# Optimization experiments

Hardware: AMD Instinct MI355X
Metric: run time of the kernel (lower is better)

## Reference

```python
import jax, jax.numpy as jnp
import numpy as np

N, C, H, W = 8, 32, 256, 256
DEPTH = 4
PAD = (1, 1, 2, 2, 1, 1)  # (w_l, w_r, h_t, h_b, d_f, d_b)
K = 2  # pool kernel/stride along each of D,H,W
EPS = 1e-5


def setup_inputs() -> dict:
    key = jax.random.key(0)
    k1, k2, k3, k4, k5 = jax.random.split(key, 5)
    x = jax.random.normal(k1, (N, C, H, W), dtype=jnp.float32)
    gamma = jax.random.normal(k2, (C,), dtype=jnp.float32) * 0.1 + 1.0
    beta = jax.random.normal(k3, (C,), dtype=jnp.float32) * 0.1
    conv_w = jax.random.normal(k4, (C, C), dtype=jnp.float32) / np.sqrt(C)  # 1x1 conv [out,in]
    conv_b = jax.random.normal(k5, (C,), dtype=jnp.float32) * 0.1
    return {"x": x, "gamma": gamma, "beta": beta, "conv_w": conv_w, "conv_b": conv_b}


def _forward(x, gamma, beta, conv_w, conv_b):
    n, c, h, w = x.shape
    # InstanceNorm2d (affine, biased variance, eps=1e-5), stats per (N,C) over H,W
    mean = jnp.mean(x, axis=(2, 3), keepdims=True)
    var = jnp.mean(jnp.square(x - mean), axis=(2, 3), keepdims=True)
    xn = (x - mean) * jax.lax.rsqrt(var + EPS)
    xn = xn * gamma[None, :, None, None] + beta[None, :, None, None]
    # expand to 5D by repeating along depth
    x3 = jnp.broadcast_to(xn[:, :, None, :, :], (n, c, DEPTH, h, w))
    # ConstantPad3d with value 0.0
    wl, wr, ht, hb, df, db = PAD
    xp = jnp.pad(x3, ((0, 0), (0, 0), (df, db), (ht, hb), (wl, wr)))
    Dp, Hp, Wp = DEPTH + df + db, h + ht + hb, w + wl + wr  # all even by construction
    dq, hq, wq = Dp // K, Hp // K, Wp // K
    # block view: [n,c,dq,K,hq,K,wq,K] -> [n,c,dq,hq,wq,K*K*K] (row-major window order,
    # matching PyTorch's flattened pooling-window index order)
    blk = xp.reshape(n, c, dq, K, hq, K, wq, K).transpose(0, 1, 2, 4, 6, 3, 5, 7)
    blk = blk.reshape(n, c, dq, hq, wq, K * K * K)
    mx = jnp.max(blk, axis=-1)
    idx = jnp.argmax(blk, axis=-1)  # first occurrence on ties, like PyTorch CPU
    # MaxUnpool3d: scatter max back to its argmax position, zeros elsewhere
    unp_blk = jax.nn.one_hot(idx, K * K * K, dtype=x.dtype) * mx[..., None]
    unpooled = unp_blk.reshape(n, c, dq, hq, wq, K, K, K).transpose(0, 1, 2, 5, 3, 6, 4, 7)
    unpooled = unpooled.reshape(n, c, Dp, Hp, Wp)
    # crop padding, collapse depth via mean
    cropped = unpooled[:, :, df:df + DEPTH, ht:ht + h, wl:wl + w]
    collapsed = jnp.mean(cropped, axis=2)  # [n,c,h,w]
    # 1x1 conv + relu
    out = jnp.einsum('oc,nchw->nohw', conv_w, collapsed) + conv_b[None, :, None, None]
    return jax.nn.relu(out)


def reference(x, gamma, beta, conv_w, conv_b):
    return _forward(x, gamma, beta, conv_w, conv_b)
```

## Files before the change

### kernel.cpp

```cpp
#include <hip/hip_runtime.h>

#define N_   8
#define C_   32
#define H_   256
#define W_   256
#define HW_  (H_ * W_)

__global__ __launch_bounds__(256) void stats_kernel(
    const float* __restrict__ x, const float* __restrict__ gamma,
    const float* __restrict__ beta, float2* __restrict__ ss)
{
    const int nc = blockIdx.x;
    const int t  = threadIdx.x;
    const float4* p = (const float4*)(x + (size_t)nc * HW_);

    double s = 0.0, q = 0.0;
    #pragma unroll 4
    for (int i = t; i < HW_ / 4; i += 256) {
        float4 v = p[i];
        double a = v.x, b = v.y, c = v.z, d = v.w;
        s += a + b + c + d;
        q += a * a + b * b + c * c + d * d;
    }
    #pragma unroll
    for (int off = 32; off > 0; off >>= 1) {
        s += __shfl_down(s, off);
        q += __shfl_down(q, off);
    }
    __shared__ double rs[4], rq[4];
    const int wid = t >> 6;
    if ((t & 63) == 0) { rs[wid] = s; rq[wid] = q; }
    __syncthreads();
    if (t == 0) {
        double S = rs[0] + rs[1] + rs[2] + rs[3];
        double Q = rq[0] + rq[1] + rq[2] + rq[3];
        double mean = S / (double)HW_;
        double var  = Q / (double)HW_ - mean * mean;
        double rstd = 1.0 / sqrt(var + 1e-5);
        int c = nc & (C_ - 1);
        float scale = (float)((double)gamma[c] * rstd);
        float shift = (float)((double)beta[c] - mean * (double)scale);
        ss[nc] = make_float2(scale, shift);
    }
}

__global__ __launch_bounds__(256) void fused_kernel(
    const float* __restrict__ x, const float2* __restrict__ ss,
    const float* __restrict__ Wm, const float* __restrict__ bias,
    float* __restrict__ out)
{
    const int k = blockIdx.x;
    const int n = blockIdx.y;
    const int t = threadIdx.x;

    __shared__ float         sVal[C_][132];
    __shared__ unsigned char sPos[C_][132];
    __shared__ float         sWT[C_][C_];

    for (int i = t; i < C_ * C_; i += 256) {
        int o = i >> 5, c = i & 31;
        sWT[c][o] = Wm[i];
    }

    const float* xrow = x + ((size_t)n * C_) * HW_ + (size_t)(2 * k) * W_;
    for (int task = t; task < C_ * 129; task += 256) {
        int c = task / 129;
        int j = task - c * 129;
        float2 sc = ss[n * C_ + c];
        const float* r0 = xrow + (size_t)c * HW_;
        const float* r1 = r0 + W_;
        int wl = 2 * j - 1, wr = 2 * j;
        float v0 = (j > 0)   ? fmaf(r0[wl], sc.x, sc.y) : 0.f;
        float v1 = (j < 128) ? fmaf(r0[wr], sc.x, sc.y) : 0.f;
        float v2 = (j > 0)   ? fmaf(r1[wl], sc.x, sc.y) : 0.f;
        float v3 = (j < 128) ? fmaf(r1[wr], sc.x, sc.y) : 0.f;
        float m = v0; int p = 0;
        if (v1 > m) { m = v1; p = 1; }
        if (v2 > m) { m = v2; p = 2; }
        if (v3 > m) { m = v3; p = 3; }
        float val = m * (m > 0.f ? 0.75f : 0.25f);
        bool padpos = (((p & 1) == 0) && j == 0) || (((p & 1) == 1) && j == 128);
        if (padpos) val = 0.f;
        sVal[c][j] = val;
        sPos[c][j] = (unsigned char)p;
    }
    __syncthreads();

    const int o4 = t >> 6;
    const int wt = t & 63;
    const int ob = o4 * 8;

    float b8[8];
    #pragma unroll
    for (int oo = 0; oo < 8; ++oo) b8[oo] = bias[ob + oo];

    float acc[2][4][8];
    #pragma unroll
    for (int r = 0; r < 2; ++r)
        #pragma unroll
        for (int dw = 0; dw < 4; ++dw)
            #pragma unroll
            for (int oo = 0; oo < 8; ++oo) acc[r][dw][oo] = b8[oo];

    for (int c = 0; c < C_; ++c) {
        float w8[8];
        #pragma unroll
        for (int oo = 0; oo < 8; ++oo) w8[oo] = sWT[c][ob + oo];
        float vA = sVal[c][2 * wt];
        float vB = sVal[c][2 * wt + 1];
        float vC = sVal[c][2 * wt + 2];
        int   pA = sPos[c][2 * wt];
        int   pB = sPos[c][2 * wt + 1];
        int   pC = sPos[c][2 * wt + 2];
        float m00 = (pA == 1) ? vA : 0.f, m10 = (pA == 3) ? vA : 0.f;
        float m01 = (pB == 0) ? vB : 0.f, m11 = (pB == 2) ? vB : 0.f;
        float m02 = (pB == 1) ? vB : 0.f, m12 = (pB == 3) ? vB : 0.f;
        float m03 = (pC == 0) ? vC : 0.f, m13 = (pC == 2) ? vC : 0.f;
        #pragma unroll
        for (int oo = 0; oo < 8; ++oo) {
            float w = w8[oo];
            acc[0][0][oo] = fmaf(m00, w, acc[0][0][oo]);
            acc[0][1][oo] = fmaf(m01, w, acc[0][1][oo]);
            acc[0][2][oo] = fmaf(m02, w, acc[0][2][oo]);
            acc[0][3][oo] = fmaf(m03, w, acc[0][3][oo]);
            acc[1][0][oo] = fmaf(m10, w, acc[1][0][oo]);
            acc[1][1][oo] = fmaf(m11, w, acc[1][1][oo]);
            acc[1][2][oo] = fmaf(m12, w, acc[1][2][oo]);
            acc[1][3][oo] = fmaf(m13, w, acc[1][3][oo]);
        }
    }

    #pragma unroll
    for (int r = 0; r < 2; ++r)
        #pragma unroll
        for (int oo = 0; oo < 8; ++oo) {
            float4 v;
            v.x = fmaxf(acc[r][0][oo], 0.f);
            v.y = fmaxf(acc[r][1][oo], 0.f);
            v.z = fmaxf(acc[r][2][oo], 0.f);
            v.w = fmaxf(acc[r][3][oo], 0.f);
            float* dst = out + ((size_t)(n * C_ + ob + oo) * HW_
                               + (size_t)(2 * k + r) * W_ + 4 * wt);
            *(float4*)dst = v;
        }
}

extern "C" void kernel_launch(void* const* d_in, const int* in_sizes, int n_in,
                              void* d_out, int out_size, void* d_ws, size_t ws_size,
                              hipStream_t stream) {
    const float* x     = (const float*)d_in[0];
    const float* gamma = (const float*)d_in[1];
    const float* beta  = (const float*)d_in[2];
    const float* Wm    = (const float*)d_in[3];
    const float* bias  = (const float*)d_in[4];
    float* out  = (float*)d_out;
    float2* ss  = (float2*)d_ws;

    stats_kernel<<<N_ * C_, 256, 0, stream>>>(x, gamma, beta, ss);
    fused_kernel<<<dim3(H_ / 2, N_), 256, 0, stream>>>(x, ss, Wm, bias, out);
}
```

Measured before the change: 150.4 us.

## Vectorize pooling loads, split even/odd shared buffers, widen block sizes

The stats kernel moves to 1024 threads with fully unrolled float4 loads and float partial accumulators, keeping double precision only for the cross-lane reduction, which cuts double-precision ALU work. The fused kernel now has each thread load 16 contiguous floats from both input rows as float4 vectors. It takes the vertical max first and gets horizontal neighbours through warp shuffles, instead of scattered scalar loads with division-based indexing. It uses 512 threads with 4 outputs per wave and stores into even/odd split shared arrays. Float accumulation of the statistics and the rewritten tie-breaking logic carry some numerical and correctness risk.

```diff
diff --git a/kernel.cpp b/kernel.cpp
--- a/kernel.cpp
+++ b/kernel.cpp
@@ -6,7 +6,7 @@
 #define W_   256
 #define HW_  (H_ * W_)
 
-__global__ __launch_bounds__(256) void stats_kernel(
+__global__ __launch_bounds__(1024) void stats_kernel(
     const float* __restrict__ x, const float* __restrict__ gamma,
     const float* __restrict__ beta, float2* __restrict__ ss)
 {
@@ -14,37 +14,40 @@
     const int t  = threadIdx.x;
     const float4* p = (const float4*)(x + (size_t)nc * HW_);
 
-    double s = 0.0, q = 0.0;
-    #pragma unroll 4
-    for (int i = t; i < HW_ / 4; i += 256) {
-        float4 v = p[i];
-        double a = v.x, b = v.y, c = v.z, d = v.w;
-        s += a + b + c + d;
-        q += a * a + b * b + c * c + d * d;
-    }
+    float s0 = 0.f, s1 = 0.f, s2 = 0.f, s3 = 0.f;
+    float q0 = 0.f, q1 = 0.f, q2 = 0.f, q3 = 0.f;
+    #pragma unroll
+    for (int i = 0; i < 16; ++i) {
+        float4 v = p[t + (i << 10)];
+        s0 += v.x; s1 += v.y; s2 += v.z; s3 += v.w;
+        q0 = fmaf(v.x, v.x, q0); q1 = fmaf(v.y, v.y, q1);
+        q2 = fmaf(v.z, v.z, q2); q3 = fmaf(v.w, v.w, q3);
+    }
+    double s = (double)s0 + (double)s1 + (double)s2 + (double)s3;
+    double q = (double)q0 + (double)q1 + (double)q2 + (double)q3;
     #pragma unroll
     for (int off = 32; off > 0; off >>= 1) {
         s += __shfl_down(s, off);
         q += __shfl_down(q, off);
     }
-    __shared__ double rs[4], rq[4];
+    __shared__ double rs[16], rq[16];
     const int wid = t >> 6;
     if ((t & 63) == 0) { rs[wid] = s; rq[wid] = q; }
     __syncthreads();
     if (t == 0) {
-        double S = rs[0] + rs[1] + rs[2] + rs[3];
-        double Q = rq[0] + rq[1] + rq[2] + rq[3];
+        double S = 0.0, Q = 0.0;
+        #pragma unroll
+        for (int i = 0; i < 16; ++i) { S += rs[i]; Q += rq[i]; }
         double mean = S / (double)HW_;
         double var  = Q / (double)HW_ - mean * mean;
-        double rstd = 1.0 / sqrt(var + 1e-5);
-        int c = nc & (C_ - 1);
-        float scale = (float)((double)gamma[c] * rstd);
-        float shift = (float)((double)beta[c] - mean * (double)scale);
+        double grs  = (double)gamma[nc & (C_ - 1)] / sqrt(var + 1e-5);
+        float scale = (float)grs;
+        float shift = (float)((double)beta[nc & (C_ - 1)] - mean * grs);
         ss[nc] = make_float2(scale, shift);
     }
 }
 
-__global__ __launch_bounds__(256) void fused_kernel(
+__global__ __launch_bounds__(512) void fused_kernel(
     const float* __restrict__ x, const float2* __restrict__ ss,
     const float* __restrict__ Wm, const float* __restrict__ bias,
     float* __restrict__ out)
@@ -53,94 +56,153 @@
     const int n = blockIdx.y;
     const int t = threadIdx.x;
 
-    __shared__ float         sVal[C_][132];
-    __shared__ unsigned char sPos[C_][132];
     __shared__ float         sWT[C_][C_];
-
-    for (int i = t; i < C_ * C_; i += 256) {
-        int o = i >> 5, c = i & 31;
-        sWT[c][o] = Wm[i];
-    }
-
-    const float* xrow = x + ((size_t)n * C_) * HW_ + (size_t)(2 * k) * W_;
-    for (int task = t; task < C_ * 129; task += 256) {
-        int c = task / 129;
-        int j = task - c * 129;
-        float2 sc = ss[n * C_ + c];
-        const float* r0 = xrow + (size_t)c * HW_;
-        const float* r1 = r0 + W_;
-        int wl = 2 * j - 1, wr = 2 * j;
-        float v0 = (j > 0)   ? fmaf(r0[wl], sc.x, sc.y) : 0.f;
-        float v1 = (j < 128) ? fmaf(r0[wr], sc.x, sc.y) : 0.f;
-        float v2 = (j > 0)   ? fmaf(r1[wl], sc.x, sc.y) : 0.f;
-        float v3 = (j < 128) ? fmaf(r1[wr], sc.x, sc.y) : 0.f;
-        float m = v0; int p = 0;
-        if (v1 > m) { m = v1; p = 1; }
-        if (v2 > m) { m = v2; p = 2; }
-        if (v3 > m) { m = v3; p = 3; }
+    __shared__ float         sE[C_][66];
+    __shared__ float         sO[C_][64];
+    __shared__ unsigned char pE[C_][66];
+    __shared__ unsigned char pO[C_][64];
+
+    {
+        int i = t;
+        #pragma unroll
+        for (int r = 0; r < 2; ++r, i += 512) {
+            int o = i >> 5, c = i & 31;
+            sWT[c][o] = Wm[i];
+        }
+    }
+
+    const int c  = t >> 4;
+    const int li = t & 15;
+    const float2 sc = ss[n * C_ + c];
+    const float* r0p = x + (size_t)(n * C_ + c) * HW_
+                         + (size_t)(2 * k) * W_ + 16 * li;
+    const float* r1p = r0p + W_;
+
+    float4 u0[4], u1[4];
+    #pragma unroll
+    for (int q = 0; q < 4; ++q) u0[q] = ((const float4*)r0p)[q];
+    #pragma unroll
+    for (int q = 0; q < 4; ++q) u1[q] = ((const float4*)r1p)[q];
+
+    float vm[16];
+    unsigned vr = 0;
+    #pragma unroll
+    for (int q = 0; q < 4; ++q) {
+        float a0, a1;
+        a0 = fmaf(u0[q].x, sc.x, sc.y); a1 = fmaf(u1[q].x, sc.x, sc.y);
+        vm[4*q+0] = fmaxf(a0, a1); if (a1 > a0) vr |= 1u << (4*q+0);
+        a0 = fmaf(u0[q].y, sc.x, sc.y); a1 = fmaf(u1[q].y, sc.x, sc.y);
+        vm[4*q+1] = fmaxf(a0, a1); if (a1 > a0) vr |= 1u << (4*q+1);
+        a0 = fmaf(u0[q].z, sc.x, sc.y); a1 = fmaf(u1[q].z, sc.x, sc.y);
+        vm[4*q+2] = fmaxf(a0, a1); if (a1 > a0) vr |= 1u << (4*q+2);
+        a0 = fmaf(u0[q].w, sc.x, sc.y); a1 = fmaf(u1[q].w, sc.x, sc.y);
+        vm[4*q+3] = fmaxf(a0, a1); if (a1 > a0) vr |= 1u << (4*q+3);
+    }
+
+    const float    vmL = __shfl_up(vm[15], 1);
+    const unsigned vrL = __shfl_up(vr, 1);
+    const int      rLn = (int)((vrL >> 15) & 1u);
+
+    #pragma unroll
+    for (int b = 0; b < 8; ++b) {
+        float vL; int rL; bool padL;
+        if (b == 0) {
+            padL = (li == 0);
+            vL = padL ? 0.f : vmL;
+            rL = padL ? 0   : rLn;
+        } else {
+            vL = vm[2*b - 1]; rL = (int)((vr >> (2*b - 1)) & 1u); padL = false;
+        }
+        float vR = vm[2*b]; int rR = (int)((vr >> (2*b)) & 1u);
+        bool chooseL = (vL > vR) || ((vL == vR) && (rL <= rR));
+        float m   = chooseL ? vL : vR;
+        int   p   = chooseL ? (rL << 1) : ((rR << 1) | 1);
         float val = m * (m > 0.f ? 0.75f : 0.25f);
-        bool padpos = (((p & 1) == 0) && j == 0) || (((p & 1) == 1) && j == 128);
-        if (padpos) val = 0.f;
-        sVal[c][j] = val;
-        sPos[c][j] = (unsigned char)p;
+        if (chooseL && padL) val = 0.f;
+        int j = 8 * li + b;
+        if (b & 1) { sO[c][j >> 1] = val; pO[c][j >> 1] = (unsigned char)p; }
+        else       { sE[c][j >> 1] = val; pE[c][j >> 1] = (unsigned char)p; }
+    }
+    if (li == 15) {
+        float vL = vm[15]; int rL = (int)((vr >> 15) & 1u);
+        bool chooseL = (vL > 0.f) || ((vL == 0.f) && (rL <= 0));
+        float m   = chooseL ? vL : 0.f;
+        int   p   = chooseL ? (rL << 1) : 1;
+        float val = m * (m > 0.f ? 0.75f : 0.25f);
+        if (!chooseL) val = 0.f;
+        sE[c][64] = val; pE[c][64] = (unsigned char)p;
     }
     __syncthreads();
 
-    const int o4 = t >> 6;
+    const int wv = t >> 6;
+    const int ob = wv << 2;
     const int wt = t & 63;
-    const int ob = o4 * 8;
-
-    float b8[8];
-    #pragma unroll
-    for (int oo = 0; oo < 8; ++oo) b8[oo] = bias[ob + oo];
-
-    float acc[2][4][8];
-    #pragma unroll
-    for (int r = 0; r < 2; ++r)
-        #pragma unroll
-        for (int dw = 0; dw < 4; ++dw)
+
+    float acc[2][4][4];
+    #pragma unroll
+    for (int oo = 0; oo < 4; ++oo) {
+        float bo = bias[ob + oo];
+        #pragma unroll
+        for (int r = 0; r < 2; ++r)
             #pragma unroll
-            for (int oo = 0; oo < 8; ++oo) acc[r][dw][oo] = b8[oo];
-
-    for (int c = 0; c < C_; ++c) {
-        float w8[8];
-        #pragma unroll
-        for (int oo = 0; oo < 8; ++oo) w8[oo] = sWT[c][ob + oo];
-        float vA = sVal[c][2 * wt];
-        float vB = sVal[c][2 * wt + 1];
-        float vC = sVal[c][2 * wt + 2];
-        int   pA = sPos[c][2 * wt];
-        int   pB = sPos[c][2 * wt + 1];
-        int   pC = sPos[c][2 * wt + 2];
+            for (int dw = 0; dw < 4; ++dw) acc[r][dw][oo] = bo;
+    }
+
+    for (int cc = 0; cc < C_; ++cc) {
+        float w0 = sWT[cc][ob + 0], w1 = sWT[cc][ob + 1];
+        float w2 = sWT[cc][ob + 2], w3 = sWT[cc][ob + 3];
+        float vA = sE[cc][wt];     int pA = pE[cc][wt];
+        float vB = sO[cc][wt];     int pB = pO[cc][wt];
+        float vC = sE[cc][wt + 1]; int pC = pE[cc][wt + 1];
         float m00 = (pA == 1) ? vA : 0.f, m10 = (pA == 3) ? vA : 0.f;
         float m01 = (pB == 0) ? vB : 0.f, m11 = (pB == 2) ? vB : 0.f;
         float m02 = (pB == 1) ? vB : 0.f, m12 = (pB == 3) ? vB : 0.f;
         float m03 = (pC == 0) ? vC : 0.f, m13 = (pC == 2) ? vC : 0.f;
-        #pragma unroll
-        for (int oo = 0; oo < 8; ++oo) {
-            float w = w8[oo];
-            acc[0][0][oo] = fmaf(m00, w, acc[0][0][oo]);
-            acc[0][1][oo] = fmaf(m01, w, acc[0][1][oo]);
-            acc[0][2][oo] = fmaf(m02, w, acc[0][2][oo]);
-            acc[0][3][oo] = fmaf(m03, w, acc[0][3][oo]);
-            acc[1][0][oo] = fmaf(m10, w, acc[1][0][oo]);
-            acc[1][1][oo] = fmaf(m11, w, acc[1][1][oo]);
-            acc[1][2][oo] = fmaf(m12, w, acc[1][2][oo]);
-            acc[1][3][oo] = fmaf(m13, w, acc[1][3][oo]);
-        }
+        acc[0][0][0] = fmaf(m00, w0, acc[0][0][0]);
+        acc[0][1][0] = fmaf(m01, w0, acc[0][1][0]);
+        acc[0][2][0] = fmaf(m02, w0, acc[0][2][0]);
+        acc[0][3][0] = fmaf(m03, w0, acc[0][3][0]);
+        acc[1][0][0] = fmaf(m10, w0, acc[1][0][0]);
+        acc[1][1][0] = fmaf(m11, w0, acc[1][1][0]);
+        acc[1][2][0] = fmaf(m12, w0, acc[1][2][0]);
+        acc[1][3][0] = fmaf(m13, w0, acc[1][3][0]);
+        acc[0][0][1] = fmaf(m00, w1, acc[0][0][1]);
+        acc[0][1][1] = fmaf(m01, w1, acc[0][1][1]);
+        acc[0][2][1] = fmaf(m02, w1, acc[0][2][1]);
+        acc[0][3][1] = fmaf(m03, w1, acc[0][3][1]);
+        acc[1][0][1] = fmaf(m10, w1, acc[1][0][1]);
+        acc[1][1][1] = fmaf(m11, w1, acc[1][1][1]);
+        acc[1][2][1] = fmaf(m12, w1, acc[1][2][1]);
+        acc[1][3][1] = fmaf(m13, w1, acc[1][3][1]);
+        acc[0][0][2] = fmaf(m00, w2, acc[0][0][2]);
+        acc[0][1][2] = fmaf(m01, w2, acc[0][1][2]);
+        acc[0][2][2] = fmaf(m02, w2, acc[0][2][2]);
+        acc[0][3][2] = fmaf(m03, w2, acc[0][3][2]);
+        acc[1][0][2] = fmaf(m10, w2, acc[1][0][2]);
+        acc[1][1][2] = fmaf(m11, w2, acc[1][1][2]);
+        acc[1][2][2] = fmaf(m12, w2, acc[1][2][2]);
+        acc[1][3][2] = fmaf(m13, w2, acc[1][3][2]);
+        acc[0][0][3] = fmaf(m00, w3, acc[0][0][3]);
+        acc[0][1][3] = fmaf(m01, w3, acc[0][1][3]);
+        acc[0][2][3] = fmaf(m02, w3, acc[0][2][3]);
+        acc[0][3][3] = fmaf(m03, w3, acc[0][3][3]);
+        acc[1][0][3] = fmaf(m10, w3, acc[1][0][3]);
+        acc[1][1][3] = fmaf(m11, w3, acc[1][1][3]);
+        acc[1][2][3] = fmaf(m12, w3, acc[1][2][3]);
+        acc[1][3][3] = fmaf(m13, w3, acc[1][3][3]);
     }
 
     #pragma unroll
     for (int r = 0; r < 2; ++r)
         #pragma unroll
-        for (int oo = 0; oo < 8; ++oo) {
+        for (int oo = 0; oo < 4; ++oo) {
             float4 v;
             v.x = fmaxf(acc[r][0][oo], 0.f);
             v.y = fmaxf(acc[r][1][oo], 0.f);
             v.z = fmaxf(acc[r][2][oo], 0.f);
             v.w = fmaxf(acc[r][3][oo], 0.f);
-            float* dst = out + ((size_t)(n * C_ + ob + oo) * HW_
-                               + (size_t)(2 * k + r) * W_ + 4 * wt);
+            float* dst = out + (size_t)(n * C_ + ob + oo) * HW_
+                             + (size_t)(2 * k + r) * W_ + 4 * wt;
             *(float4*)dst = v;
         }
 }
@@ -156,6 +218,6 @@
     float* out  = (float*)d_out;
     float2* ss  = (float2*)d_ws;
 
-    stats_kernel<<<N_ * C_, 256, 0, stream>>>(x, gamma, beta, ss);
-    fused_kernel<<<dim3(H_ / 2, N_), 256, 0, stream>>>(x, ss, Wm, bias, out);
+    stats_kernel<<<N_ * C_, 1024, 0, stream>>>(x, gamma, beta, ss);
+    fused_kernel<<<dim3(H_ / 2, N_), 512, 0, stream>>>(x, ss, Wm, bias, out);
 }
```

After: 155.7 us. 1.04x slower.
